# Optimization experiments

Hardware: AMD Instinct MI355X
Metric: run time of the kernel (lower is better)

## Reference

```python
import jax, jax.numpy as jnp
import numpy as np
import math

HID_DIM = 1024
NUM_HEADS = 8
QK_DIM = HID_DIM // 8  # 128 total, 16 per head


def setup_inputs() -> dict:
    key = jax.random.key(0)
    ks = jax.random.split(key, 7)
    B, M, C = 4, 2048, HID_DIM
    gain = math.sqrt(2.0)  # calculate_gain('relu')

    def xavier(k, fan_in, fan_out):
        std = gain * math.sqrt(2.0 / (fan_in + fan_out))
        a = math.sqrt(3.0) * std
        return jax.random.uniform(k, (fan_out, fan_in), jnp.float32, -a, a)

    x = jax.random.normal(ks[0], (B, M, C), jnp.float32)
    Wq = xavier(ks[1], C, QK_DIM)   # [out, in] like torch Linear
    Wk = xavier(ks[2], C, QK_DIM)
    Wv = xavier(ks[3], C, C)
    bq = jnp.zeros((QK_DIM,), jnp.float32)
    bk = jnp.zeros((QK_DIM,), jnp.float32)
    bv = jnp.zeros((C,), jnp.float32)
    gamma = jnp.zeros((1,), jnp.float32)
    return {"x": x, "Wq": Wq, "bq": bq, "Wk": Wk, "bk": bk,
            "Wv": Wv, "bv": bv, "gamma": gamma}


def reference(x, Wq, bq, Wk, bk, Wv, bv, gamma):
    B, M, C = x.shape
    H = NUM_HEADS
    dqk = QK_DIM // H   # per-head qk dim = 16
    dv = C // H         # per-head v dim = 128
    q = (x @ Wq.T + bq).reshape(B, M, H, dqk)  # [B,M,H,dqk]
    k = (x @ Wk.T + bk).reshape(B, M, H, dqk)
    v = (x @ Wv.T + bv).reshape(B, M, H, dv)
    scores = jnp.einsum('bmhd,bnhd->bhmn', q, k) / math.sqrt(dqk)
    scores = jnp.where(scores >= 0, scores, 0.2 * scores)  # LeakyReLU(0.2)
    beta = jax.nn.softmax(scores, axis=-1)                 # [B,H,M,M]
    out = jnp.einsum('bhmn,bnhd->bmhd', beta, v).reshape(B, M, C)
    return gamma * out + x
```

## Files before the change

### kernel.cpp

```cpp
#include <hip/hip_runtime.h>
#include <hip/hip_bf16.h>

typedef __bf16 bf16_t;
typedef __bf16 bf16x8 __attribute__((ext_vector_type(8)));
typedef float f32x4 __attribute__((ext_vector_type(4)));
typedef float f32x16 __attribute__((ext_vector_type(16)));

#define MTOT 8192
#define CDIM 1024
#define HEADS 8
#define DV 128
#define QKD 128
#define SEQ 2048
#define QSCALE 0.3606737602222409f

struct alignas(8) B4 { bf16_t a, b, c, d; };

__device__ inline bf16x8 cvt8(float4 a, float4 b) {
    bf16x8 v = { (bf16_t)a.x, (bf16_t)a.y, (bf16_t)a.z, (bf16_t)a.w,
                 (bf16_t)b.x, (bf16_t)b.y, (bf16_t)b.z, (bf16_t)b.w };
    return v;
}

__device__ inline void gl_lds16(const bf16_t* g, bf16_t* l) {
    __builtin_amdgcn_global_load_lds(
        (const __attribute__((address_space(1))) void*)g,
        (__attribute__((address_space(3))) void*)l, 16, 0, 0);
}

__device__ inline unsigned cvtpk(float a, float b) {
    unsigned r;
    asm("v_cvt_pk_bf16_f32 %0, %1, %2" : "=v"(r) : "v"(a), "v"(b));
    return r;
}

__device__ inline void plswap(unsigned& a, unsigned& b) {
    asm("v_permlane32_swap_b32 %0, %1" : "+v"(a), "+v"(b));
}

__global__ __launch_bounds__(256) void cvt_x(
    const float* __restrict__ src, bf16_t* __restrict__ dst, int n8)
{
    int i = blockIdx.x * blockDim.x + threadIdx.x;
    if (i >= n8) return;
    const float4* s = reinterpret_cast<const float4*>(src) + (size_t)i * 2;
    reinterpret_cast<bf16x8*>(dst)[i] = cvt8(s[0], s[1]);
}

__global__ __launch_bounds__(256) void cvt_w(
    const float* __restrict__ Wq, const float* __restrict__ Wk,
    const float* __restrict__ Wv, bf16_t* __restrict__ Wb)
{
    int i = blockIdx.x * blockDim.x + threadIdx.x;
    const float* src;
    if (i < 16384)       src = Wq + (size_t)i * 8;
    else if (i < 32768)  src = Wk + (size_t)(i - 16384) * 8;
    else                 src = Wv + (size_t)(i - 32768) * 8;
    const float4* s = reinterpret_cast<const float4*>(src);
    reinterpret_cast<bf16x8*>(Wb)[i] = cvt8(s[0], s[1]);
}

__global__ __launch_bounds__(256) void qkv_gemm3(
    const bf16_t* __restrict__ Xb, const bf16_t* __restrict__ Wb,
    const float* __restrict__ bq, const float* __restrict__ bk,
    const float* __restrict__ bv,
    bf16_t* __restrict__ Qw, bf16_t* __restrict__ Kw, bf16_t* __restrict__ Vt)
{
    __shared__ bf16_t As[128][64];
    __shared__ bf16_t Bs[128][64];

    const int tid = threadIdx.x;
    const int w = tid >> 6, l = tid & 63;
    const int c = l & 15, q = l >> 4;
    const int rw = w & 1, cw = w >> 1;

    const int lin = blockIdx.x + 10 * blockIdx.y;
    const int xcd = lin & 7, jj = lin >> 3;
    const int bx = jj % 10;
    const int m0 = (xcd * 8 + jj / 10) * 128;

    const bf16_t* Arow = Xb + (size_t)(m0 + w * 8 + (l >> 3)) * CDIM + (l & 7) * 8;
    const bf16_t* Brow = Wb + (size_t)(bx * 128 + w * 8 + (l >> 3)) * CDIM + (l & 7) * 8;

    f32x4 acc[16] = {};

    for (int k0 = 0; k0 < CDIM; k0 += 64) {
        __syncthreads();
        #pragma unroll
        for (int i = 0; i < 4; ++i) {
            gl_lds16(Arow + k0 + (size_t)i * 32 * CDIM, &As[i * 32 + w * 8][0]);
            gl_lds16(Brow + k0 + (size_t)i * 32 * CDIM, &Bs[i * 32 + w * 8][0]);
        }
        __syncthreads();
        #pragma unroll
        for (int kk = 0; kk < 2; ++kk) {
            bf16x8 af[4], bfr[4];
            #pragma unroll
            for (int mt = 0; mt < 4; ++mt)
                af[mt] = *(const bf16x8*)&As[rw * 64 + mt * 16 + c][kk * 32 + q * 8];
            #pragma unroll
            for (int nt = 0; nt < 4; ++nt)
                bfr[nt] = *(const bf16x8*)&Bs[cw * 64 + nt * 16 + c][kk * 32 + q * 8];
            #pragma unroll
            for (int mt = 0; mt < 4; ++mt)
                #pragma unroll
                for (int nt = 0; nt < 4; ++nt)
                    acc[mt * 4 + nt] = __builtin_amdgcn_mfma_f32_16x16x32_bf16(
                        af[mt], bfr[nt], acc[mt * 4 + nt], 0, 0, 0);
        }
    }

    #pragma unroll
    for (int mt = 0; mt < 4; ++mt)
        #pragma unroll
        for (int nt = 0; nt < 4; ++nt) {
            const int cl = cw * 64 + nt * 16 + c;
            f32x4 a = acc[mt * 4 + nt];
            const int mg = m0 + rw * 64 + mt * 16 + q * 4;
            if (bx == 0) {
                const float bb = bq[cl];
                #pragma unroll
                for (int r = 0; r < 4; ++r)
                    Qw[(size_t)(mg + r) * QKD + cl] = (bf16_t)((a[r] + bb) * QSCALE);
            } else if (bx == 1) {
                const float bb = bk[cl];
                #pragma unroll
                for (int r = 0; r < 4; ++r)
                    Kw[(size_t)(mg + r) * QKD + cl] = (bf16_t)(a[r] + bb);
            } else {
                const int h = bx - 2;
                const float bb = bv[h * DV + cl];
                const int bidx = mg >> 11, ml = mg & 2047;
                B4 v{ (bf16_t)(a[0] + bb), (bf16_t)(a[1] + bb),
                      (bf16_t)(a[2] + bb), (bf16_t)(a[3] + bb) };
                *(B4*)(Vt + ((size_t)(bidx * HEADS + h) * DV + cl) * SEQ + ml) = v;
            }
        }
}

__global__ __launch_bounds__(256, 2) void qkv_gemm2(
    const float* __restrict__ X,
    const float* __restrict__ Wq, const float* __restrict__ bq,
    const float* __restrict__ Wk, const float* __restrict__ bk,
    const float* __restrict__ Wv, const float* __restrict__ bv,
    bf16_t* __restrict__ Qw, bf16_t* __restrict__ Kw, bf16_t* __restrict__ Vt)
{
    __shared__ alignas(16) bf16_t As[128][72];
    __shared__ alignas(16) bf16_t Bs[128][72];

    const int tid  = threadIdx.x;
    const int lane = tid & 63, wave = tid >> 6;
    const int c = lane & 15, q = lane >> 4;
    const int rw = wave & 1, cw = wave >> 1;
    const int m0 = blockIdx.y * 128;
    const int nt_idx = blockIdx.x;

    const float* W; const float* bias;
    if (nt_idx == 0)      { W = Wq; bias = bq; }
    else if (nt_idx == 1) { W = Wk; bias = bk; }
    else { W = Wv + (size_t)(nt_idx - 2) * DV * CDIM; bias = bv + (nt_idx - 2) * DV; }

    const int srow = tid >> 1, sseg = tid & 1;
    const int swr = (srow >> 3) & 3;
    const float* ax = X + (size_t)(m0 + srow) * CDIM + sseg * 32;
    const float* bxp = W + (size_t)srow * CDIM + sseg * 32;

    f32x4 acc[16] = {};

    for (int k0 = 0; k0 < CDIM; k0 += 64) {
        __syncthreads();
        #pragma unroll
        for (int i = 0; i < 4; ++i) {
            const int ph = (sseg * 4 + i) ^ swr;
            *(bf16x8*)&As[srow][ph * 8] = cvt8(*(const float4*)(ax + k0 + i * 8),
                                               *(const float4*)(ax + k0 + i * 8 + 4));
            *(bf16x8*)&Bs[srow][ph * 8] = cvt8(*(const float4*)(bxp + k0 + i * 8),
                                               *(const float4*)(bxp + k0 + i * 8 + 4));
        }
        __syncthreads();
        #pragma unroll
        for (int kk = 0; kk < 2; ++kk) {
            bf16x8 af[4], bfr[4];
            #pragma unroll
            for (int mt = 0; mt < 4; ++mt) {
                const int row = rw * 64 + mt * 16 + c;
                af[mt] = *(const bf16x8*)&As[row][((kk * 4 + q) ^ ((row >> 3) & 3)) * 8];
            }
            #pragma unroll
            for (int nt = 0; nt < 4; ++nt) {
                const int row = cw * 64 + nt * 16 + c;
                bfr[nt] = *(const bf16x8*)&Bs[row][((kk * 4 + q) ^ ((row >> 3) & 3)) * 8];
            }
            #pragma unroll
            for (int mt = 0; mt < 4; ++mt)
                #pragma unroll
                for (int nt = 0; nt < 4; ++nt)
                    acc[mt * 4 + nt] = __builtin_amdgcn_mfma_f32_16x16x32_bf16(
                        af[mt], bfr[nt], acc[mt * 4 + nt], 0, 0, 0);
        }
    }

    #pragma unroll
    for (int mt = 0; mt < 4; ++mt)
        #pragma unroll
        for (int nt = 0; nt < 4; ++nt) {
            const int col = cw * 64 + nt * 16 + c;
            const float bb = bias[col];
            f32x4 a = acc[mt * 4 + nt];
            const int mg = m0 + rw * 64 + mt * 16 + q * 4;
            if (nt_idx == 0) {
                #pragma unroll
                for (int r = 0; r < 4; ++r)
                    Qw[(size_t)(mg + r) * QKD + col] = (bf16_t)((a[r] + bb) * QSCALE);
            } else if (nt_idx == 1) {
                #pragma unroll
                for (int r = 0; r < 4; ++r)
                    Kw[(size_t)(mg + r) * QKD + col] = (bf16_t)(a[r] + bb);
            } else {
                const int h = nt_idx - 2;
                const int bidx = mg >> 11, ml = mg & 2047;
                B4 v{ (bf16_t)(a[0] + bb), (bf16_t)(a[1] + bb),
                      (bf16_t)(a[2] + bb), (bf16_t)(a[3] + bb) };
                *(B4*)(Vt + ((size_t)(bidx * HEADS + h) * DV + col) * SEQ + ml) = v;
            }
        }
}

__global__ __launch_bounds__(256, 2) void attn3(
    const bf16_t* __restrict__ Q, const bf16_t* __restrict__ K,
    const bf16_t* __restrict__ Vt, const float* __restrict__ X,
    const float* __restrict__ gptr, float* __restrict__ out)
{
    __shared__ alignas(16) bf16_t Vs[2][128][72];

    const int tid  = threadIdx.x;
    const int lane = tid & 63;
    const int c5 = lane & 31, q1 = lane >> 5;

    const int lin = blockIdx.x + (SEQ / 128) * blockIdx.y;
    const int xcd = lin & 7, jj = lin >> 3;
    const int bh = xcd * 4 + (jj >> 4);
    const int qt = jj & 15;
    const int b = bh >> 3, h = bh & 7;
    const int wave = tid >> 6;
    const int mbase = qt * 128 + wave * 32;

    const bf16x8 qf = *(const bf16x8*)(
        Q + (size_t)(b * SEQ + mbase + c5) * QKD + h * 16 + q1 * 8);

    float li = 0.f;
    f32x16 o[4] = {};

    const bf16_t* Vhead = Vt + (size_t)(b * HEADS + h) * DV * SEQ;
    const bf16_t* Kbase = K + (size_t)(b * SEQ) * QKD + h * 16;

    const int sdv = tid >> 1, sseg = tid & 1;
    const int swv = (sdv >> 3) & 7;

    bf16x8 vA[4], vB[4], kA[2], kB[2];

    {
        const bf16_t* s0 = Vhead + (size_t)sdv * SEQ + sseg * 32;
        #pragma unroll
        for (int i = 0; i < 4; ++i) vA[i] = *(const bf16x8*)(s0 + i * 8);
        const bf16_t* s1 = s0 + 64;
        #pragma unroll
        for (int i = 0; i < 4; ++i) vB[i] = *(const bf16x8*)(s1 + i * 8);
        #pragma unroll
        for (int blk = 0; blk < 2; ++blk) {
            kA[blk] = *(const bf16x8*)(Kbase + (size_t)(blk * 32 + c5) * QKD + q1 * 8);
            kB[blk] = *(const bf16x8*)(Kbase + (size_t)(64 + blk * 32 + c5) * QKD + q1 * 8);
        }
        #pragma unroll
        for (int i = 0; i < 4; ++i) {
            const int ph = (sseg * 4 + i) ^ swv;
            *(bf16x8*)&Vs[0][sdv][ph * 8] = vA[i];
        }
        const bf16_t* s2 = s0 + 128;
        #pragma unroll
        for (int i = 0; i < 4; ++i) vA[i] = *(const bf16x8*)(s2 + i * 8);
    }

    union U8 { bf16x8 v; unsigned u[4]; };

    #pragma unroll 1
    for (int t = 0; t < 32; t += 2) {
        #pragma unroll
        for (int half = 0; half < 2; ++half) {
            __syncthreads();
            #pragma unroll
            for (int i = 0; i < 4; ++i) {
                const int ph = (sseg * 4 + i) ^ swv;
                *(bf16x8*)&Vs[half ? 0 : 1][sdv][ph * 8] = half ? vA[i] : vB[i];
            }
            const int cur = t + half;
            const bf16x8 k0f = half ? kB[0] : kA[0];
            const bf16x8 k1f = half ? kB[1] : kA[1];
            {
                const int vt  = (cur + 3 < 32) ? cur + 3 : 31;
                const int kt2 = (cur + 2 < 32) ? cur + 2 : 31;
                const bf16_t* src = Vhead + (size_t)sdv * SEQ + vt * 64 + sseg * 32;
                #pragma unroll
                for (int i = 0; i < 4; ++i) {
                    bf16x8 vv = *(const bf16x8*)(src + i * 8);
                    if (half) vA[i] = vv; else vB[i] = vv;
                }
                #pragma unroll
                for (int blk = 0; blk < 2; ++blk) {
                    bf16x8 kk = *(const bf16x8*)(
                        Kbase + (size_t)(kt2 * 64 + blk * 32 + c5) * QKD + q1 * 8);
                    if (half) kB[blk] = kk; else kA[blk] = kk;
                }
            }

            U8 frag[4];
            #pragma unroll
            for (int blk = 0; blk < 2; ++blk) {
                f32x16 z = {};
                f32x16 s = __builtin_amdgcn_mfma_f32_32x32x16_bf16(
                    blk ? k1f : k0f, qf, z, 0, 0, 0);
                float e[16];
                #pragma unroll
                for (int r = 0; r < 16; ++r) {
                    const float sv = s[r];
                    const float ev = __builtin_amdgcn_exp2f(fmaxf(sv, 0.2f * sv));
                    e[r] = ev;
                    li += ev;
                }
                unsigned w0 = cvtpk(e[0], e[1]),   w1 = cvtpk(e[2], e[3]);
                unsigned w2 = cvtpk(e[4], e[5]),   w3 = cvtpk(e[6], e[7]);
                unsigned w4 = cvtpk(e[8], e[9]),   w5 = cvtpk(e[10], e[11]);
                unsigned w6 = cvtpk(e[12], e[13]), w7 = cvtpk(e[14], e[15]);
                plswap(w0, w2); plswap(w1, w3);
                plswap(w4, w6); plswap(w5, w7);
                frag[blk * 2 + 0].u[0] = w0; frag[blk * 2 + 0].u[1] = w1;
                frag[blk * 2 + 0].u[2] = w2; frag[blk * 2 + 0].u[3] = w3;
                frag[blk * 2 + 1].u[0] = w4; frag[blk * 2 + 1].u[1] = w5;
                frag[blk * 2 + 1].u[2] = w6; frag[blk * 2 + 1].u[3] = w7;
            }

            __builtin_amdgcn_s_setprio(1);
            #pragma unroll
            for (int kt = 0; kt < 4; ++kt) {
                const bf16x8 pa = frag[kt].v;
                #pragma unroll
                for (int dvt = 0; dvt < 4; ++dvt) {
                    const int dv = dvt * 32 + c5;
                    const int phB = (kt * 2 + q1) ^ ((dv >> 3) & 7);
                    const bf16x8 vb = *(const bf16x8*)&Vs[half][dv][phB * 8];
                    o[dvt] = __builtin_amdgcn_mfma_f32_32x32x16_bf16(
                        pa, vb, o[dvt], 0, 0, 0);
                }
            }
            __builtin_amdgcn_s_setprio(0);
        }
    }

    li += __shfl_xor(li, 32);
    const float inv = 1.f / li;
    const float g = gptr[0];

    #pragma unroll
    for (int dvt = 0; dvt < 4; ++dvt)
        #pragma unroll
        for (int r = 0; r < 16; ++r) {
            const int row = (r & 3) + 8 * (r >> 2) + 4 * q1;
            const float linv = __shfl(inv, row);
            const size_t idx = (size_t)(b * SEQ + mbase + row) * CDIM
                             + h * DV + dvt * 32 + c5;
            out[idx] = g * (o[dvt][r] * linv) + X[idx];
        }
}

extern "C" void kernel_launch(void* const* d_in, const int* in_sizes, int n_in,
                              void* d_out, int out_size, void* d_ws, size_t ws_size,
                              hipStream_t stream) {
    const float* X  = (const float*)d_in[0];
    const float* Wq = (const float*)d_in[1];
    const float* bq = (const float*)d_in[2];
    const float* Wk = (const float*)d_in[3];
    const float* bk = (const float*)d_in[4];
    const float* Wv = (const float*)d_in[5];
    const float* bv = (const float*)d_in[6];
    const float* g  = (const float*)d_in[7];
    float* out = (float*)d_out;

    dim3 blk(256);
    const size_t big_elems = (size_t)MTOT * CDIM + 1280 * CDIM
                           + (size_t)MTOT * QKD * 2 + (size_t)MTOT * CDIM;
    const size_t big_ws = big_elems * sizeof(bf16_t);

    if (ws_size >= big_ws) {
        bf16_t* Xb = (bf16_t*)d_ws;
        bf16_t* Wb = Xb + (size_t)MTOT * CDIM;
        bf16_t* Qw = Wb + (size_t)1280 * CDIM;
        bf16_t* Kw = Qw + (size_t)MTOT * QKD;
        bf16_t* Vt = Kw + (size_t)MTOT * QKD;

        hipLaunchKernelGGL(cvt_x, dim3(MTOT * CDIM / 8 / 256), blk, 0, stream,
                           X, Xb, MTOT * CDIM / 8);
        hipLaunchKernelGGL(cvt_w, dim3(1280 * CDIM / 8 / 256), blk, 0, stream,
                           Wq, Wk, Wv, Wb);
        hipLaunchKernelGGL(qkv_gemm3, dim3(10, 64), blk, 0, stream,
                           Xb, Wb, bq, bk, bv, Qw, Kw, Vt);
        hipLaunchKernelGGL(attn3, dim3(SEQ / 128, 32), blk, 0, stream,
                           Qw, Kw, Vt, X, g, out);
    } else {
        bf16_t* Qw = (bf16_t*)d_ws;
        bf16_t* Kw = Qw + (size_t)MTOT * QKD;
        bf16_t* Vt = Kw + (size_t)MTOT * QKD;
        hipLaunchKernelGGL(qkv_gemm2, dim3(10, 64), blk, 0, stream,
                           X, Wq, bq, Wk, bk, Wv, bv, Qw, Kw, Vt);
        hipLaunchKernelGGL(attn3, dim3(SEQ / 128, 32), blk, 0, stream,
                           Qw, Kw, Vt, X, g, out);
    }
}
```

Measured before the change: 205.8 us.

## Merge conversion kernels, drop GEMM XCD swizzle, compute softmax denominator via MFMA

Measured after the change: 206.1 us. Within noise of the previous version (+0.2%).

```diff
diff --git a/kernel.cpp b/kernel.cpp
--- a/kernel.cpp
+++ b/kernel.cpp
@@ -38,26 +38,28 @@
     asm("v_permlane32_swap_b32 %0, %1" : "+v"(a), "+v"(b));
 }
 
-__global__ __launch_bounds__(256) void cvt_x(
-    const float* __restrict__ src, bf16_t* __restrict__ dst, int n8)
+#define XITEMS (MTOT * CDIM / 8)
+#define WITEMS (1280 * CDIM / 8)
+
+__global__ __launch_bounds__(256) void cvt_all(
+    const float* __restrict__ X,
+    const float* __restrict__ Wq, const float* __restrict__ Wk,
+    const float* __restrict__ Wv,
+    bf16_t* __restrict__ Xb, bf16_t* __restrict__ Wb)
 {
     int i = blockIdx.x * blockDim.x + threadIdx.x;
-    if (i >= n8) return;
-    const float4* s = reinterpret_cast<const float4*>(src) + (size_t)i * 2;
-    reinterpret_cast<bf16x8*>(dst)[i] = cvt8(s[0], s[1]);
-}
-
-__global__ __launch_bounds__(256) void cvt_w(
-    const float* __restrict__ Wq, const float* __restrict__ Wk,
-    const float* __restrict__ Wv, bf16_t* __restrict__ Wb)
-{
-    int i = blockIdx.x * blockDim.x + threadIdx.x;
-    const float* src;
-    if (i < 16384)       src = Wq + (size_t)i * 8;
-    else if (i < 32768)  src = Wk + (size_t)(i - 16384) * 8;
-    else                 src = Wv + (size_t)(i - 32768) * 8;
-    const float4* s = reinterpret_cast<const float4*>(src);
-    reinterpret_cast<bf16x8*>(Wb)[i] = cvt8(s[0], s[1]);
+    if (i < XITEMS) {
+        const float4* s = reinterpret_cast<const float4*>(X) + (size_t)i * 2;
+        reinterpret_cast<bf16x8*>(Xb)[i] = cvt8(s[0], s[1]);
+    } else {
+        int j = i - XITEMS;
+        const float* src;
+        if (j < 16384)       src = Wq + (size_t)j * 8;
+        else if (j < 32768)  src = Wk + (size_t)(j - 16384) * 8;
+        else                 src = Wv + (size_t)(j - 32768) * 8;
+        const float4* s = reinterpret_cast<const float4*>(src);
+        reinterpret_cast<bf16x8*>(Wb)[j] = cvt8(s[0], s[1]);
+    }
 }
 
 __global__ __launch_bounds__(256) void qkv_gemm3(
@@ -73,11 +75,8 @@
     const int w = tid >> 6, l = tid & 63;
     const int c = l & 15, q = l >> 4;
     const int rw = w & 1, cw = w >> 1;
-
-    const int lin = blockIdx.x + 10 * blockIdx.y;
-    const int xcd = lin & 7, jj = lin >> 3;
-    const int bx = jj % 10;
-    const int m0 = (xcd * 8 + jj / 10) * 128;
+    const int bx = blockIdx.x;
+    const int m0 = blockIdx.y * 128;
 
     const bf16_t* Arow = Xb + (size_t)(m0 + w * 8 + (l >> 3)) * CDIM + (l & 7) * 8;
     const bf16_t* Brow = Wb + (size_t)(bx * 128 + w * 8 + (l >> 3)) * CDIM + (l & 7) * 8;
@@ -248,8 +247,11 @@
     const bf16x8 qf = *(const bf16x8*)(
         Q + (size_t)(b * SEQ + mbase + c5) * QKD + h * 16 + q1 * 8);
 
-    float li = 0.f;
+    const bf16x8 ones = { (bf16_t)1.0f, (bf16_t)1.0f, (bf16_t)1.0f, (bf16_t)1.0f,
+                          (bf16_t)1.0f, (bf16_t)1.0f, (bf16_t)1.0f, (bf16_t)1.0f };
+
     f32x16 o[4] = {};
+    f32x16 oli = {};
 
     const bf16_t* Vhead = Vt + (size_t)(b * HEADS + h) * DV * SEQ;
     const bf16_t* Kbase = K + (size_t)(b * SEQ) * QKD + h * 16;
@@ -323,9 +325,7 @@
                 #pragma unroll
                 for (int r = 0; r < 16; ++r) {
                     const float sv = s[r];
-                    const float ev = __builtin_amdgcn_exp2f(fmaxf(sv, 0.2f * sv));
-                    e[r] = ev;
-                    li += ev;
+                    e[r] = __builtin_amdgcn_exp2f(fmaxf(sv, 0.2f * sv));
                 }
                 unsigned w0 = cvtpk(e[0], e[1]),   w1 = cvtpk(e[2], e[3]);
                 unsigned w2 = cvtpk(e[4], e[5]),   w3 = cvtpk(e[6], e[7]);
@@ -351,25 +351,25 @@
                     o[dvt] = __builtin_amdgcn_mfma_f32_32x32x16_bf16(
                         pa, vb, o[dvt], 0, 0, 0);
                 }
+                oli = __builtin_amdgcn_mfma_f32_32x32x16_bf16(pa, ones, oli, 0, 0, 0);
             }
             __builtin_amdgcn_s_setprio(0);
         }
     }
 
-    li += __shfl_xor(li, 32);
-    const float inv = 1.f / li;
     const float g = gptr[0];
 
     #pragma unroll
-    for (int dvt = 0; dvt < 4; ++dvt)
-        #pragma unroll
-        for (int r = 0; r < 16; ++r) {
-            const int row = (r & 3) + 8 * (r >> 2) + 4 * q1;
-            const float linv = __shfl(inv, row);
+    for (int r = 0; r < 16; ++r) {
+        const int row = (r & 3) + 8 * (r >> 2) + 4 * q1;
+        const float inv = 1.f / oli[r];
+        #pragma unroll
+        for (int dvt = 0; dvt < 4; ++dvt) {
             const size_t idx = (size_t)(b * SEQ + mbase + row) * CDIM
                              + h * DV + dvt * 32 + c5;
-            out[idx] = g * (o[dvt][r] * linv) + X[idx];
-        }
+            out[idx] = g * (o[dvt][r] * inv) + X[idx];
+        }
+    }
 }
 
 extern "C" void kernel_launch(void* const* d_in, const int* in_sizes, int n_in,
@@ -397,10 +397,8 @@
         bf16_t* Kw = Qw + (size_t)MTOT * QKD;
         bf16_t* Vt = Kw + (size_t)MTOT * QKD;
 
-        hipLaunchKernelGGL(cvt_x, dim3(MTOT * CDIM / 8 / 256), blk, 0, stream,
-                           X, Xb, MTOT * CDIM / 8);
-        hipLaunchKernelGGL(cvt_w, dim3(1280 * CDIM / 8 / 256), blk, 0, stream,
-                           Wq, Wk, Wv, Wb);
+        hipLaunchKernelGGL(cvt_all, dim3((XITEMS + WITEMS) / 256), blk, 0, stream,
+                           X, Wq, Wk, Wv, Xb, Wb);
         hipLaunchKernelGGL(qkv_gemm3, dim3(10, 64), blk, 0, stream,
                            Xb, Wb, bq, bk, bv, Qw, Kw, Vt);
         hipLaunchKernelGGL(attn3, dim3(SEQ / 128, 32), blk, 0, stream,
```
